# Kernel tuning notes

Measured on AMD Instinct MI355X. Metric: run time of the kernel, lower is better.

## Reference

```python
import jax, jax.numpy as jnp
import numpy as np

ALPHA = 0.2
N_ENT, N_TYP, N_REL, E = 100000, 1000, 200, 500000
D = 64          # nfeat1 = nfeat2 = nhid1 = nhid2 = relation_dim
NHEADS = 2      # forced by the tuple-unpack in the original forward


def _xavier(key, shape):
    fan_out, fan_in = shape[0], shape[-1]
    lim = 1.414 * np.sqrt(6.0 / (fan_in + fan_out))
    return jax.random.uniform(key, shape, jnp.float32, -lim, lim)


def setup_inputs() -> dict:
    key = jax.random.key(0)
    ks = jax.random.split(key, 32)
    inp = {
        "entity_embeddings": jax.random.normal(ks[0], (N_ENT, D), jnp.float32),
        "type_embed": jax.random.normal(ks[1], (N_TYP, D), jnp.float32),
        "relation_embed": jax.random.normal(ks[2], (N_REL, D), jnp.float32),
        "edge_list": jax.random.randint(ks[3], (2, E), 0, N_TYP),  # row0=src entity, row1=dst type; both in-range
        "edge_type": jax.random.randint(ks[4], (E,), 0, N_REL),
        "edge_embed": jax.random.normal(ks[5], (E, D), jnp.float32),
    }
    Din = 3 * D  # cat(x1[src], x2[dst], edge_embed)
    i = 6
    for h in range(NHEADS):
        inp[f"a_e{h}"] = _xavier(ks[i], (D, Din)); i += 1   # entity-side attention proj
        inp[f"v_e{h}"] = _xavier(ks[i], (1, D))[0]; i += 1  # entity-side score vector
        inp[f"a_t{h}"] = _xavier(ks[i], (D, Din)); i += 1   # type-side attention proj
        inp[f"v_t{h}"] = _xavier(ks[i], (1, D))[0]; i += 1
    Ho = NHEADS * D       # 128
    Dout = 3 * Ho         # out layer input cat dim
    inp["a_eo"] = _xavier(ks[i], (Ho, Dout)); i += 1
    inp["v_eo"] = _xavier(ks[i], (1, Ho))[0]; i += 1
    inp["a_to"] = _xavier(ks[i], (Ho, Dout)); i += 1
    inp["v_to"] = _xavier(ks[i], (1, Ho))[0]; i += 1
    inp["W"] = _xavier(ks[i], (D, Ho))  # relation_dim -> nheads*nhid1
    return inp


def _gat_e2t(x1, x2, src, dst, e, a_e, v_e, a_t, v_t, concat):
    """Bipartite sparse GAT layer (KBGAT-style, e2t variant).
    Message m = a @ cat(x1[src], x2[dst], edge_embed); score = exp(-leaky_relu(v . m));
    softmax-normalized scatter-aggregate to entity nodes (by src) and type nodes (by dst)."""
    d1, d2 = x1.shape[1], x2.shape[1]

    def agg(a, v, seg, nseg):
        a1, a2, a3 = a[:, :d1], a[:, d1:d1 + d2], a[:, d1 + d2:]
        # project nodes first, then gather (avoids materializing [E, 3d] cat)
        m = (x1 @ a1.T)[src] + (x2 @ a2.T)[dst] + e @ a3.T     # [E, h]
        s = jnp.exp(-jax.nn.leaky_relu(m @ v, ALPHA))          # [E] unnormalized attention
        num = jax.ops.segment_sum(m * s[:, None], seg, num_segments=nseg)
        den = jax.ops.segment_sum(s, seg, num_segments=nseg)
        h = num / jnp.where(den == 0, 1.0, den)[:, None]
        return jax.nn.elu(h) if concat else h

    h_e = agg(a_e, v_e, src, x1.shape[0])
    h_t = agg(a_t, v_t, dst, x2.shape[0])
    return h_e, h_t


def reference(entity_embeddings, type_embed, relation_embed, edge_list, edge_type, edge_embed,
              a_e0, v_e0, a_t0, v_t0, a_e1, v_e1, a_t1, v_t1,
              a_eo, v_eo, a_to, v_to, W):
    src, dst = edge_list[0], edge_list[1]
    # two attention heads (concat=True -> elu inside)
    h0e, h0t = _gat_e2t(entity_embeddings, type_embed, src, dst, edge_embed, a_e0, v_e0, a_t0, v_t0, True)
    h1e, h1t = _gat_e2t(entity_embeddings, type_embed, src, dst, edge_embed, a_e1, v_e1, a_t1, v_t1, True)
    x1 = jnp.concatenate([h0e, h1e], axis=1)  # [N_ENT, 2*nhid1]
    x2 = jnp.concatenate([h0t, h1t], axis=1)  # [N_TYP, 2*nhid2]
    # dropout is identity at inference
    out_rel = relation_embed @ W              # [N_REL, nheads*nhid1]
    e2 = out_rel[edge_type]                   # per-edge relation embedding
    o1, o2 = _gat_e2t(x1, x2, src, dst, e2, a_eo, v_eo, a_to, v_to, False)
    return jax.nn.elu(o1), jax.nn.elu(o2), out_rel
```

## Files before the change

kernel.cpp:

```cpp
#include <hip/hip_runtime.h>

#define ALPHA 0.2f
#define NT 1000
#define NRELC 200
#define NE 500000
#define N_ENT 100000
#define CH 4096
#define G 123

static constexpr size_t I_STARTS_SRC = 0;
static constexpr size_t I_STARTS_DST = 1001;
static constexpr size_t I_COLSUM     = 2002;
static constexpr size_t I_HIST2      = 4002;
static constexpr size_t I_BASE2      = 250002;
static constexpr size_t I_AB_SRC     = 496002;
static constexpr size_t I_AB_DST     = 1496002;

static constexpr size_t F_U1 = 2496004;
static constexpr size_t F_U2 = F_U1 + 768;
static constexpr size_t F_L1 = F_U2 + 768;
static constexpr size_t F_X1 = F_L1 + 4*130000;
static constexpr size_t F_X2 = F_X1 + 128000;
static constexpr size_t F_OR = F_X2 + 128000;
static constexpr size_t F_L2 = F_OR + 25600;
static constexpr size_t S2F = 283800;
static constexpr size_t WS_FLOATS = F_L2 + 2*S2F;

static constexpr size_t OUT_O2  = 12800000;
static constexpr size_t OUT_REL = 12928000;

__device__ __forceinline__ float eluf(float x) { return x > 0.f ? x : expm1f(x); }
__device__ __forceinline__ float scoref(float slin) {
  return expf(slin > 0.f ? -slin : -ALPHA * slin);
}

__global__ __launch_bounds__(256) void k_hist2(const int* __restrict__ src,
                                               const int* __restrict__ dst,
                                               int* __restrict__ ip) {
  __shared__ int h[NT];
  int bid = blockIdx.x;
  int side = bid >= G;
  int blk = bid - side * G;
  const int* keys = side ? dst : src;
  int j0 = blk * CH;
  int n = min(CH, NE - j0);
  for (int i = threadIdx.x; i < NT; i += 256) h[i] = 0;
  __syncthreads();
  for (int k = threadIdx.x; k < n; k += 256) atomicAdd(&h[keys[j0 + k]], 1);
  __syncthreads();
  int* row = ip + I_HIST2 + (size_t)(side * G + blk) * NT;
  for (int b = threadIdx.x; b < NT; b += 256) row[b] = h[b];
}

__global__ void k_colsum(int* __restrict__ ip) {
  int t = blockIdx.x * 256 + threadIdx.x;
  if (t >= 2 * NT) return;
  int side = t / NT, bin = t - side * NT;
  int s = 0;
  for (int blk = 0; blk < G; ++blk)
    s += ip[I_HIST2 + (size_t)(side * G + blk) * NT + bin];
  ip[I_COLSUM + t] = s;
}

__global__ void k_scan2b(int* __restrict__ ip) {
  __shared__ int buf[1024];
  int t = threadIdx.x;
  for (int side = 0; side < 2; ++side) {
    int v = (t < NT) ? ip[I_COLSUM + side * NT + t] : 0;
    buf[t] = v;
    __syncthreads();
    for (int off = 1; off < 1024; off <<= 1) {
      int x = (t >= off) ? buf[t - off] : 0;
      __syncthreads();
      buf[t] += x;
      __syncthreads();
    }
    int* st = ip + (side ? I_STARTS_DST : I_STARTS_SRC);
    if (t < NT) st[t] = buf[t] - v;
    if (t == NT - 1) st[NT] = buf[t];
    __syncthreads();
  }
}

__global__ void k_bases(int* __restrict__ ip) {
  int t = blockIdx.x * 256 + threadIdx.x;
  if (t >= 2 * NT) return;
  int side = t / NT, bin = t - side * NT;
  int run = ip[(side ? I_STARTS_DST : I_STARTS_SRC) + bin];
  for (int blk = 0; blk < G; ++blk) {
    size_t idx = I_HIST2 + (size_t)(side * G + blk) * NT + bin;
    int c = ip[idx];
    ip[idx + (I_BASE2 - I_HIST2)] = run;
    run += c;
  }
}

__global__ __launch_bounds__(256) void k_binscat(const int* __restrict__ src,
                                                 const int* __restrict__ dst,
                                                 const int* __restrict__ et,
                                                 int* __restrict__ ip) {
  __shared__ int2 bufs[CH];
  __shared__ int loff[1024];
  __shared__ int lcur[1024];
  __shared__ int gbase[1024];
  __shared__ int psum[256];
  int bid = blockIdx.x;
  int side = bid >= G;
  int blk = bid - side * G;
  const int* keys = side ? dst : src;
  const int* oths = side ? src : dst;
  int j0 = blk * CH;
  int n = min(CH, NE - j0);
  int t = threadIdx.x;

  for (int i = t; i < 1024; i += 256) lcur[i] = 0;
  __syncthreads();
  for (int k = t; k < n; k += 256) atomicAdd(&lcur[keys[j0 + k]], 1);
  __syncthreads();
  int c0 = lcur[4*t], c1 = lcur[4*t+1], c2 = lcur[4*t+2], c3 = lcur[4*t+3];
  int s = c0 + c1 + c2 + c3;
  psum[t] = s;
  __syncthreads();
  for (int off = 1; off < 256; off <<= 1) {
    int x = (t >= off) ? psum[t - off] : 0;
    __syncthreads();
    psum[t] += x;
    __syncthreads();
  }
  int base = psum[t] - s;
  loff[4*t]   = base;
  loff[4*t+1] = base + c0;
  loff[4*t+2] = base + c0 + c1;
  loff[4*t+3] = base + c0 + c1 + c2;
  lcur[4*t]   = loff[4*t];
  lcur[4*t+1] = loff[4*t+1];
  lcur[4*t+2] = loff[4*t+2];
  lcur[4*t+3] = loff[4*t+3];
  const int* brow = ip + I_BASE2 + (size_t)(side * G + blk) * NT;
  for (int b = t; b < NT; b += 256) gbase[b] = brow[b];
  __syncthreads();
  for (int k = t; k < n; k += 256) {
    int j = j0 + k;
    int b = keys[j];
    int pos = atomicAdd(&lcur[b], 1);
    bufs[pos] = make_int2(j | (b << 19), oths[j] | (et[j] << 16));
  }
  __syncthreads();
  int2* out = reinterpret_cast<int2*>(ip + (side ? I_AB_DST : I_AB_SRC));
  for (int k = t; k < n; k += 256) {
    int2 q = bufs[k];
    int b = q.x >> 19;
    int posg = gbase[b] + (k - loff[b]);
    out[posg] = make_int2(q.x & 0x7FFFF, q.y);
  }
}

__global__ void k_prep_u(const float* aE0, const float* vE0, const float* aT0, const float* vT0,
                         const float* aE1, const float* vE1, const float* aT1, const float* vT1,
                         const float* aEo, const float* vEo, const float* aTo, const float* vTo,
                         float* ws) {
  int t = blockIdx.x * blockDim.x + threadIdx.x;
  if (t < 768) {
    int c = t / 192, rem = t - c*192;
    int p = rem >> 6, k = rem & 63;
    const float* a = (c==0)?aE0:(c==1)?aT0:(c==2)?aE1:aT1;
    const float* v = (c==0)?vE0:(c==1)?vT0:(c==2)?vE1:vT1;
    float s = 0.f;
    for (int o = 0; o < 64; ++o) s += a[o*192 + p*64 + k] * v[o];
    ws[F_U1 + (size_t)(c*3+p)*64 + k] = s;
  } else if (t < 1536) {
    int tt = t - 768;
    int c = tt / 384, rem = tt - c*384;
    int p = rem >> 7, k = rem & 127;
    const float* a = c ? aTo : aEo;
    const float* v = c ? vTo : vEo;
    float s = 0.f;
    for (int o = 0; o < 128; ++o) s += a[o*384 + p*128 + k] * v[o];
    ws[F_U2 + (size_t)(c*3+p)*128 + k] = s;
  }
}

__global__ void k_l1_proj(const float* Ent, const float* Typ,
                          const float* aE0, const float* aT0,
                          const float* aE1, const float* aT1,
                          float* ws) {
  int stride = gridDim.x * blockDim.x;
  for (int t = blockIdx.x * blockDim.x + threadIdx.x; t < 4*130000; t += stride) {
    int c = t / 130000, rem = t - c*130000;
    const float* a = (c==0)?aE0:(c==1)?aT0:(c==2)?aE1:aT1;
    float* base = ws + F_L1 + (size_t)c * 130000;
    if (rem < 64000) {
      int i = rem >> 6, o = rem & 63;
      const float* x = Ent + (size_t)i*64;
      const float* ar = a + o*192;
      float s = 0.f;
      #pragma unroll
      for (int k = 0; k < 64; ++k) s += x[k]*ar[k];
      base[rem] = s;
    } else if (rem < 128000) {
      int rr = rem - 64000; int i = rr >> 6, o = rr & 63;
      const float* x = Typ + (size_t)i*64;
      const float* ar = a + o*192 + 64;
      float s = 0.f;
      #pragma unroll
      for (int k = 0; k < 64; ++k) s += x[k]*ar[k];
      base[64000 + rr] = s;
    } else if (rem < 129000) {
      int i = rem - 128000;
      const float* x = Ent + (size_t)i*64;
      const float* u = ws + F_U1 + (size_t)(c*3)*64;
      float s = 0.f;
      #pragma unroll
      for (int k = 0; k < 64; ++k) s += x[k]*u[k];
      base[128000 + i] = s;
    } else {
      int i = rem - 129000;
      const float* x = Typ + (size_t)i*64;
      const float* u = ws + F_U1 + (size_t)(c*3+1)*64;
      float s = 0.f;
      #pragma unroll
      for (int k = 0; k < 64; ++k) s += x[k]*u[k];
      base[129000 + i] = s;
    }
  }
}

__global__ __launch_bounds__(256) void k_l1_acc(const float* __restrict__ Eemb,
                                                const float* aE0, const float* aT0,
                                                const float* aE1, const float* aT1,
                                                const int* __restrict__ ip,
                                                float* __restrict__ ws) {
  __shared__ float Tl[2][NT];
  __shared__ float cOthL[2][NT];
  __shared__ float accR[2][16][64];
  __shared__ float accE[2][64];
  __shared__ float red[256];
  __shared__ float denl[2];

  int side = blockIdx.x >= NT;
  int g = blockIdx.x - side * NT;
  int t = threadIdx.x;
  int sub = t & 15, slot = t >> 4;
  int c0 = side, c1 = side + 2;

  size_t othOff = side ? 128000 : 129000;
  size_t ownOff = side ? 129000 : 128000;
  for (int i = t; i < NT; i += 256) {
    Tl[0][i] = 0.f; Tl[1][i] = 0.f;
    cOthL[0][i] = ws[F_L1 + (size_t)c0*130000 + othOff + i];
    cOthL[1][i] = ws[F_L1 + (size_t)c1*130000 + othOff + i];
  }
  if (t < 2) denl[t] = 0.f;
  float ownA = ws[F_L1 + (size_t)c0*130000 + ownOff + g];
  float ownB = ws[F_L1 + (size_t)c1*130000 + ownOff + g];
  float4 w3A = reinterpret_cast<const float4*>(ws + F_U1 + (size_t)(c0*3+2)*64)[sub];
  float4 w3B = reinterpret_cast<const float4*>(ws + F_U1 + (size_t)(c1*3+2)*64)[sub];
  __syncthreads();

  int start = ip[(side ? I_STARTS_DST : I_STARTS_SRC) + g];
  int end   = ip[(side ? I_STARTS_DST : I_STARTS_SRC) + g + 1];
  const int2* ab = reinterpret_cast<const int2*>(ip + (side ? I_AB_DST : I_AB_SRC));
  const float4* EV = reinterpret_cast<const float4*>(Eemb);

  float4 acc0 = make_float4(0.f,0.f,0.f,0.f);
  float4 acc1 = make_float4(0.f,0.f,0.f,0.f);
  float d0 = 0.f, d1 = 0.f;

  int p = start + slot;
  for (; p + 48 < end; p += 64) {
    int2 q0 = ab[p], q1 = ab[p+16], q2 = ab[p+32], q3 = ab[p+48];
    float4 e0 = EV[(size_t)q0.x*16 + sub];
    float4 e1 = EV[(size_t)q1.x*16 + sub];
    float4 e2 = EV[(size_t)q2.x*16 + sub];
    float4 e3 = EV[(size_t)q3.x*16 + sub];
    float rA0 = e0.x*w3A.x + e0.y*w3A.y + e0.z*w3A.z + e0.w*w3A.w;
    float rB0 = e0.x*w3B.x + e0.y*w3B.y + e0.z*w3B.z + e0.w*w3B.w;
    float rA1 = e1.x*w3A.x + e1.y*w3A.y + e1.z*w3A.z + e1.w*w3A.w;
    float rB1 = e1.x*w3B.x + e1.y*w3B.y + e1.z*w3B.z + e1.w*w3B.w;
    float rA2 = e2.x*w3A.x + e2.y*w3A.y + e2.z*w3A.z + e2.w*w3A.w;
    float rB2 = e2.x*w3B.x + e2.y*w3B.y + e2.z*w3B.z + e2.w*w3B.w;
    float rA3 = e3.x*w3A.x + e3.y*w3A.y + e3.z*w3A.z + e3.w*w3A.w;
    float rB3 = e3.x*w3B.x + e3.y*w3B.y + e3.z*w3B.z + e3.w*w3B.w;
    #pragma unroll
    for (int sh = 1; sh < 16; sh <<= 1) {
      rA0 += __shfl_xor(rA0, sh, 16); rB0 += __shfl_xor(rB0, sh, 16);
      rA1 += __shfl_xor(rA1, sh, 16); rB1 += __shfl_xor(rB1, sh, 16);
      rA2 += __shfl_xor(rA2, sh, 16); rB2 += __shfl_xor(rB2, sh, 16);
      rA3 += __shfl_xor(rA3, sh, 16); rB3 += __shfl_xor(rB3, sh, 16);
    }
    int o0 = q0.y & 0xFFFF, o1 = q1.y & 0xFFFF, o2 = q2.y & 0xFFFF, o3 = q3.y & 0xFFFF;
    float sA0 = scoref(ownA + cOthL[0][o0] + rA0);
    float sB0 = scoref(ownB + cOthL[1][o0] + rB0);
    float sA1 = scoref(ownA + cOthL[0][o1] + rA1);
    float sB1 = scoref(ownB + cOthL[1][o1] + rB1);
    float sA2 = scoref(ownA + cOthL[0][o2] + rA2);
    float sB2 = scoref(ownB + cOthL[1][o2] + rB2);
    float sA3 = scoref(ownA + cOthL[0][o3] + rA3);
    float sB3 = scoref(ownB + cOthL[1][o3] + rB3);
    acc0.x += sA0*e0.x + sA1*e1.x + sA2*e2.x + sA3*e3.x;
    acc0.y += sA0*e0.y + sA1*e1.y + sA2*e2.y + sA3*e3.y;
    acc0.z += sA0*e0.z + sA1*e1.z + sA2*e2.z + sA3*e3.z;
    acc0.w += sA0*e0.w + sA1*e1.w + sA2*e2.w + sA3*e3.w;
    acc1.x += sB0*e0.x + sB1*e1.x + sB2*e2.x + sB3*e3.x;
    acc1.y += sB0*e0.y + sB1*e1.y + sB2*e2.y + sB3*e3.y;
    acc1.z += sB0*e0.z + sB1*e1.z + sB2*e2.z + sB3*e3.z;
    acc1.w += sB0*e0.w + sB1*e1.w + sB2*e2.w + sB3*e3.w;
    if (sub == 0) {
      atomicAdd(&Tl[0][o0], sA0); atomicAdd(&Tl[1][o0], sB0);
      atomicAdd(&Tl[0][o1], sA1); atomicAdd(&Tl[1][o1], sB1);
      atomicAdd(&Tl[0][o2], sA2); atomicAdd(&Tl[1][o2], sB2);
      atomicAdd(&Tl[0][o3], sA3); atomicAdd(&Tl[1][o3], sB3);
      d0 += sA0 + sA1 + sA2 + sA3;
      d1 += sB0 + sB1 + sB2 + sB3;
    }
  }
  for (; p < end; p += 16) {
    int2 q = ab[p];
    float4 ev = EV[(size_t)q.x*16 + sub];
    float rA = ev.x*w3A.x + ev.y*w3A.y + ev.z*w3A.z + ev.w*w3A.w;
    float rB = ev.x*w3B.x + ev.y*w3B.y + ev.z*w3B.z + ev.w*w3B.w;
    #pragma unroll
    for (int sh = 1; sh < 16; sh <<= 1) {
      rA += __shfl_xor(rA, sh, 16);
      rB += __shfl_xor(rB, sh, 16);
    }
    int oth = q.y & 0xFFFF;
    float sA = scoref(ownA + cOthL[0][oth] + rA);
    float sB = scoref(ownB + cOthL[1][oth] + rB);
    acc0.x += sA*ev.x; acc0.y += sA*ev.y; acc0.z += sA*ev.z; acc0.w += sA*ev.w;
    acc1.x += sB*ev.x; acc1.y += sB*ev.y; acc1.z += sB*ev.z; acc1.w += sB*ev.w;
    if (sub == 0) {
      atomicAdd(&Tl[0][oth], sA);
      atomicAdd(&Tl[1][oth], sB);
      d0 += sA; d1 += sB;
    }
  }
  *reinterpret_cast<float4*>(&accR[0][slot][sub*4]) = acc0;
  *reinterpret_cast<float4*>(&accR[1][slot][sub*4]) = acc1;
  if (sub == 0) { atomicAdd(&denl[0], d0); atomicAdd(&denl[1], d1); }
  __syncthreads();
  if (t < 128) {
    int ci = t >> 6, o = t & 63;
    float s = 0.f;
    #pragma unroll
    for (int sl = 0; sl < 16; ++sl) s += accR[ci][sl][o];
    accE[ci][o] = s;
  }
  __syncthreads();

  int o = t & 63, part = t >> 6;
  size_t othPOff = side ? 0 : 64000;
  size_t ownPOff = side ? 64000 : 0;
  #pragma unroll
  for (int ci = 0; ci < 2; ++ci) {
    int c = side + 2*ci;
    const float* Pc = ws + F_L1 + (size_t)c * 130000;
    const float* Poth = Pc + othPOff;
    float sum = 0.f;
    for (int dd = part*250; dd < part*250 + 250; ++dd)
      sum += Tl[ci][dd] * Poth[(size_t)dd*64 + o];
    red[t] = sum;
    __syncthreads();
    if (part == 0) {
      sum = red[o] + red[64+o] + red[128+o] + red[192+o];
      const float* a = (c==0)?aE0:(c==1)?aT0:(c==2)?aE1:aT1;
      const float* a3 = a + o*192 + 128;
      float acc = 0.f;
      #pragma unroll
      for (int k = 0; k < 64; ++k) acc += accE[ci][k]*a3[k];
      float den = denl[ci];
      float own = Pc[ownPOff + (size_t)g*64 + o];
      float num = sum + acc + den*own;
      float h = num / (den == 0.f ? 1.f : den);
      float* dst = ws + (side ? F_X2 : F_X1);
      dst[(size_t)g*128 + ci*64 + o] = eluf(h);
    }
    __syncthreads();
  }
}

__global__ void k_relW(const float* Rel, const float* W, float* ws, float* dout) {
  int t = blockIdx.x * blockDim.x + threadIdx.x;
  if (t >= NRELC*128) return;
  int r = t >> 7, o = t & 127;
  const float* x = Rel + (size_t)r*64;
  float s = 0.f;
  #pragma unroll
  for (int k = 0; k < 64; ++k) s += x[k] * W[(size_t)k*128 + o];
  ws[F_OR + t] = s;
  dout[OUT_REL + t] = s;
}

__global__ void k_l2_proj(const float* aEo, const float* aTo, float* ws) {
  int stride = gridDim.x * blockDim.x;
  const float* x1 = ws + F_X1;
  const float* x2 = ws + F_X2;
  const float* orel = ws + F_OR;
  for (int t = blockIdx.x * blockDim.x + threadIdx.x; t < 2*283800; t += stride) {
    int c = t / 283800, rem = t - c*283800;
    const float* a = c ? aTo : aEo;
    float* base = ws + F_L2 + (size_t)c * S2F;
    if (rem < 128000) {
      int i = rem >> 7, o = rem & 127;
      const float* x = x1 + (size_t)i*128;
      const float* ar = a + (size_t)o*384;
      float s = 0.f;
      #pragma unroll
      for (int k = 0; k < 128; ++k) s += x[k]*ar[k];
      base[rem] = s;
    } else if (rem < 256000) {
      int rr = rem - 128000; int i = rr >> 7, o = rr & 127;
      const float* x = x2 + (size_t)i*128;
      const float* ar = a + (size_t)o*384 + 128;
      float s = 0.f;
      #pragma unroll
      for (int k = 0; k < 128; ++k) s += x[k]*ar[k];
      base[128000 + rr] = s;
    } else if (rem < 281600) {
      int rr = rem - 256000; int r = rr >> 7, o = rr & 127;
      const float* x = orel + (size_t)r*128;
      const float* ar = a + (size_t)o*384 + 256;
      float s = 0.f;
      #pragma unroll
      for (int k = 0; k < 128; ++k) s += x[k]*ar[k];
      base[256000 + rr] = s;
    } else if (rem < 282600) {
      int i = rem - 281600;
      const float* u = ws + F_U2 + (size_t)(c*3)*128;
      const float* x = x1 + (size_t)i*128;
      float s = 0.f;
      for (int k = 0; k < 128; ++k) s += x[k]*u[k];
      base[281600 + i] = s;
    } else if (rem < 283600) {
      int i = rem - 282600;
      const float* u = ws + F_U2 + (size_t)(c*3+1)*128;
      const float* x = x2 + (size_t)i*128;
      float s = 0.f;
      for (int k = 0; k < 128; ++k) s += x[k]*u[k];
      base[282600 + i] = s;
    } else {
      int r = rem - 283600;
      const float* u = ws + F_U2 + (size_t)(c*3+2)*128;
      const float* x = orel + (size_t)r*128;
      float s = 0.f;
      for (int k = 0; k < 128; ++k) s += x[k]*u[k];
      base[283600 + r] = s;
    }
  }
}

__global__ __launch_bounds__(256) void k_l2_seg(const int* __restrict__ ip,
                                                float* __restrict__ ws,
                                                float* __restrict__ dout) {
  __shared__ float Tl[NT];
  __shared__ float Ul[NRELC];
  __shared__ float cOthL[NT];
  __shared__ float cRelL[NRELC];
  __shared__ float red[256];
  __shared__ float denl;

  int c = blockIdx.x >= NT;
  int g = blockIdx.x - c * NT;
  int t = threadIdx.x;
  float* base = ws + F_L2 + (size_t)c * S2F;

  size_t othOff = c ? 281600 : 282600;
  size_t ownOff = c ? 282600 : 281600;
  for (int i = t; i < NT; i += 256) { Tl[i] = 0.f; cOthL[i] = base[othOff + i]; }
  for (int i = t; i < NRELC; i += 256) { Ul[i] = 0.f; cRelL[i] = base[283600 + i]; }
  if (t == 0) denl = 0.f;
  float own = base[ownOff + g];
  __syncthreads();

  int start = ip[(c ? I_STARTS_DST : I_STARTS_SRC) + g];
  int end   = ip[(c ? I_STARTS_DST : I_STARTS_SRC) + g + 1];
  const int2* ab = reinterpret_cast<const int2*>(ip + (c ? I_AB_DST : I_AB_SRC));

  float dpart = 0.f;
  for (int p = start + t; p < end; p += 256) {
    int2 q = ab[p];
    int oth = q.y & 0xFFFF;
    int r = q.y >> 16;
    float sv = scoref(own + cOthL[oth] + cRelL[r]);
    atomicAdd(&Tl[oth], sv);
    atomicAdd(&Ul[r], sv);
    dpart += sv;
  }
  atomicAdd(&denl, dpart);
  __syncthreads();

  int o = t & 127, part = t >> 7;
  const float* Qoth = base + (c ? 0 : 128000);
  const float* R3 = base + 256000;
  float sum = 0.f;
  for (int dd = part*500; dd < part*500 + 500; ++dd)
    sum += Tl[dd] * Qoth[(size_t)dd*128 + o];
  for (int rr = part*100; rr < part*100 + 100; ++rr)
    sum += Ul[rr] * R3[(size_t)rr*128 + o];
  red[t] = sum;
  __syncthreads();
  if (part == 0) {
    sum = red[o] + red[128+o];
    float den = denl;
    float ownQ = base[(c ? 128000 : 0) + (size_t)g*128 + o];
    float num = sum + den*ownQ;
    float h = num / (den == 0.f ? 1.f : den);
    size_t off = c ? (OUT_O2 + (size_t)g*128 + o) : ((size_t)g*128 + o);
    dout[off] = eluf(h);
  }
}

extern "C" void kernel_launch(void* const* d_in, const int* in_sizes, int n_in,
                              void* d_out, int out_size, void* d_ws, size_t ws_size,
                              hipStream_t stream) {
  (void)in_sizes; (void)n_in;
  const float* Ent = (const float*)d_in[0];
  const float* Typ = (const float*)d_in[1];
  const float* Rel = (const float*)d_in[2];
  const int*   edge = (const int*)d_in[3];
  const int*   etyp = (const int*)d_in[4];
  const float* Eemb = (const float*)d_in[5];
  const float* aE0 = (const float*)d_in[6];
  const float* vE0 = (const float*)d_in[7];
  const float* aT0 = (const float*)d_in[8];
  const float* vT0 = (const float*)d_in[9];
  const float* aE1 = (const float*)d_in[10];
  const float* vE1 = (const float*)d_in[11];
  const float* aT1 = (const float*)d_in[12];
  const float* vT1 = (const float*)d_in[13];
  const float* aEo = (const float*)d_in[14];
  const float* vEo = (const float*)d_in[15];
  const float* aTo = (const float*)d_in[16];
  const float* vTo = (const float*)d_in[17];
  const float* W   = (const float*)d_in[18];
  float* ws  = (float*)d_ws;
  int*   ip  = (int*)d_ws;
  float* out = (float*)d_out;
  const int* srcA = edge;
  const int* dstA = edge + NE;

  if (ws_size < WS_FLOATS * sizeof(float)) return;

  hipMemsetAsync(d_out, 0, (size_t)out_size * sizeof(float), stream);

  k_hist2  <<<2*G, 256, 0, stream>>>(srcA, dstA, ip);
  k_colsum <<<8, 256, 0, stream>>>(ip);
  k_scan2b <<<1, 1024, 0, stream>>>(ip);
  k_bases  <<<8, 256, 0, stream>>>(ip);
  k_binscat<<<2*G, 256, 0, stream>>>(srcA, dstA, etyp, ip);
  k_prep_u <<<6, 256, 0, stream>>>(aE0,vE0,aT0,vT0,aE1,vE1,aT1,vT1,aEo,vEo,aTo,vTo,ws);
  k_l1_proj<<<2048, 256, 0, stream>>>(Ent, Typ, aE0, aT0, aE1, aT1, ws);
  k_l1_acc <<<2000, 256, 0, stream>>>(Eemb, aE0, aT0, aE1, aT1, ip, ws);
  k_relW   <<<100, 256, 0, stream>>>(Rel, W, ws, out);
  k_l2_proj<<<2218, 256, 0, stream>>>(aEo, aTo, ws);
  k_l2_seg <<<2000, 256, 0, stream>>>(ip, ws, out);
}
```

Before: 303.6 us.

## Tile node projection kernels with shared-memory row tiles and register blocking

Rewrites the layer-1 and layer-2 node projection kernels so that each block stages a 16-row tile of node features in shared memory. Each thread then computes 4 or 8 output rows for one output column, reusing each weight element across those rows. The scalar u-vector dot products move to a separate tail range of blocks. This is meant to cut redundant global loads of features and weights, at the cost of fewer blocks and more register pressure.

Result: faster. 262.5 us (-13.6%).

```diff
diff --git a/kernel.cpp b/kernel.cpp
--- a/kernel.cpp
+++ b/kernel.cpp
@@ -180,41 +180,56 @@
   }
 }
 
-__global__ void k_l1_proj(const float* Ent, const float* Typ,
-                          const float* aE0, const float* aT0,
-                          const float* aE1, const float* aT1,
-                          float* ws) {
-  int stride = gridDim.x * blockDim.x;
-  for (int t = blockIdx.x * blockDim.x + threadIdx.x; t < 4*130000; t += stride) {
-    int c = t / 130000, rem = t - c*130000;
+__global__ __launch_bounds__(256) void k_l1_proj(const float* Ent, const float* Typ,
+                                                 const float* aE0, const float* aT0,
+                                                 const float* aE1, const float* aT1,
+                                                 float* ws) {
+  int bid = blockIdx.x;
+  int t = threadIdx.x;
+  if (bid < 504) {
+    __shared__ float xs[16][64];
+    int c = bid / 126, rem = bid - c*126;
+    int table = rem / 63, tile = rem - table*63;
+    int i0 = tile * 16;
     const float* a = (c==0)?aE0:(c==1)?aT0:(c==2)?aE1:aT1;
+    const float* x = table ? Typ : Ent;
+    float* outb = ws + F_L1 + (size_t)c*130000 + (table ? 64000 : 0);
+    for (int idx = t; idx < 1024; idx += 256) {
+      int r = idx >> 6, k = idx & 63;
+      int i = i0 + r;
+      xs[r][k] = (i < NT) ? x[(size_t)i*64 + k] : 0.f;
+    }
+    __syncthreads();
+    int o = t & 63, grp = t >> 6;
+    const float* arow = a + o*192 + table*64;
+    float acc0 = 0.f, acc1 = 0.f, acc2 = 0.f, acc3 = 0.f;
+    #pragma unroll 8
+    for (int k = 0; k < 64; ++k) {
+      float av = arow[k];
+      acc0 += xs[grp*4+0][k] * av;
+      acc1 += xs[grp*4+1][k] * av;
+      acc2 += xs[grp*4+2][k] * av;
+      acc3 += xs[grp*4+3][k] * av;
+    }
+    int ib = i0 + grp*4;
+    if (ib + 0 < NT) outb[(size_t)(ib+0)*64 + o] = acc0;
+    if (ib + 1 < NT) outb[(size_t)(ib+1)*64 + o] = acc1;
+    if (ib + 2 < NT) outb[(size_t)(ib+2)*64 + o] = acc2;
+    if (ib + 3 < NT) outb[(size_t)(ib+3)*64 + o] = acc3;
+  } else {
+    int idx = (bid - 504) * 256 + t;
+    if (idx >= 8000) return;
+    int c = idx / 2000, rem = idx - c*2000;
     float* base = ws + F_L1 + (size_t)c * 130000;
-    if (rem < 64000) {
-      int i = rem >> 6, o = rem & 63;
-      const float* x = Ent + (size_t)i*64;
-      const float* ar = a + o*192;
-      float s = 0.f;
-      #pragma unroll
-      for (int k = 0; k < 64; ++k) s += x[k]*ar[k];
-      base[rem] = s;
-    } else if (rem < 128000) {
-      int rr = rem - 64000; int i = rr >> 6, o = rr & 63;
-      const float* x = Typ + (size_t)i*64;
-      const float* ar = a + o*192 + 64;
-      float s = 0.f;
-      #pragma unroll
-      for (int k = 0; k < 64; ++k) s += x[k]*ar[k];
-      base[64000 + rr] = s;
-    } else if (rem < 129000) {
-      int i = rem - 128000;
-      const float* x = Ent + (size_t)i*64;
+    if (rem < 1000) {
+      const float* x = Ent + (size_t)rem*64;
       const float* u = ws + F_U1 + (size_t)(c*3)*64;
       float s = 0.f;
       #pragma unroll
       for (int k = 0; k < 64; ++k) s += x[k]*u[k];
-      base[128000 + i] = s;
+      base[128000 + rem] = s;
     } else {
-      int i = rem - 129000;
+      int i = rem - 1000;
       const float* x = Typ + (size_t)i*64;
       const float* u = ws + F_U1 + (size_t)(c*3+1)*64;
       float s = 0.f;
@@ -391,55 +406,63 @@
   dout[OUT_REL + t] = s;
 }
 
-__global__ void k_l2_proj(const float* aEo, const float* aTo, float* ws) {
-  int stride = gridDim.x * blockDim.x;
+__global__ __launch_bounds__(256) void k_l2_proj(const float* aEo, const float* aTo,
+                                                 float* ws) {
+  int bid = blockIdx.x;
+  int t = threadIdx.x;
   const float* x1 = ws + F_X1;
   const float* x2 = ws + F_X2;
   const float* orel = ws + F_OR;
-  for (int t = blockIdx.x * blockDim.x + threadIdx.x; t < 2*283800; t += stride) {
-    int c = t / 283800, rem = t - c*283800;
+  if (bid < 278) {
+    __shared__ float xs[16][128];
+    int c = bid / 139, rem = bid - c*139;
     const float* a = c ? aTo : aEo;
+    float* cb = ws + F_L2 + (size_t)c * S2F;
+    const float* x; int part, tile, nrows; float* outb;
+    if (rem < 63)       { x = x1;   part = 0; tile = rem;       nrows = NT;    outb = cb; }
+    else if (rem < 126) { x = x2;   part = 1; tile = rem - 63;  nrows = NT;    outb = cb + 128000; }
+    else                { x = orel; part = 2; tile = rem - 126; nrows = NRELC; outb = cb + 256000; }
+    int i0 = tile * 16;
+    for (int idx = t; idx < 2048; idx += 256) {
+      int r = idx >> 7, k = idx & 127;
+      int i = i0 + r;
+      xs[r][k] = (i < nrows) ? x[(size_t)i*128 + k] : 0.f;
+    }
+    __syncthreads();
+    int o = t & 127, grp = t >> 7;
+    const float* arow = a + (size_t)o*384 + part*128;
+    float acc[8] = {0.f,0.f,0.f,0.f,0.f,0.f,0.f,0.f};
+    #pragma unroll 4
+    for (int k = 0; k < 128; ++k) {
+      float av = arow[k];
+      #pragma unroll
+      for (int r = 0; r < 8; ++r)
+        acc[r] += xs[grp*8+r][k] * av;
+    }
+    int ib = i0 + grp*8;
+    #pragma unroll
+    for (int r = 0; r < 8; ++r)
+      if (ib + r < nrows) outb[(size_t)(ib+r)*128 + o] = acc[r];
+  } else {
+    int idx = (bid - 278) * 256 + t;
+    if (idx >= 4400) return;
+    int c = idx / 2200, rem = idx - c*2200;
     float* base = ws + F_L2 + (size_t)c * S2F;
-    if (rem < 128000) {
-      int i = rem >> 7, o = rem & 127;
-      const float* x = x1 + (size_t)i*128;
-      const float* ar = a + (size_t)o*384;
-      float s = 0.f;
-      #pragma unroll
-      for (int k = 0; k < 128; ++k) s += x[k]*ar[k];
-      base[rem] = s;
-    } else if (rem < 256000) {
-      int rr = rem - 128000; int i = rr >> 7, o = rr & 127;
-      const float* x = x2 + (size_t)i*128;
-      const float* ar = a + (size_t)o*384 + 128;
-      float s = 0.f;
-      #pragma unroll
-      for (int k = 0; k < 128; ++k) s += x[k]*ar[k];
-      base[128000 + rr] = s;
-    } else if (rem < 281600) {
-      int rr = rem - 256000; int r = rr >> 7, o = rr & 127;
-      const float* x = orel + (size_t)r*128;
-      const float* ar = a + (size_t)o*384 + 256;
-      float s = 0.f;
-      #pragma unroll
-      for (int k = 0; k < 128; ++k) s += x[k]*ar[k];
-      base[256000 + rr] = s;
-    } else if (rem < 282600) {
-      int i = rem - 281600;
+    if (rem < 1000) {
       const float* u = ws + F_U2 + (size_t)(c*3)*128;
-      const float* x = x1 + (size_t)i*128;
+      const float* x = x1 + (size_t)rem*128;
       float s = 0.f;
       for (int k = 0; k < 128; ++k) s += x[k]*u[k];
-      base[281600 + i] = s;
-    } else if (rem < 283600) {
-      int i = rem - 282600;
+      base[281600 + rem] = s;
+    } else if (rem < 2000) {
+      int i = rem - 1000;
       const float* u = ws + F_U2 + (size_t)(c*3+1)*128;
       const float* x = x2 + (size_t)i*128;
       float s = 0.f;
       for (int k = 0; k < 128; ++k) s += x[k]*u[k];
       base[282600 + i] = s;
     } else {
-      int r = rem - 283600;
+      int r = rem - 2000;
       const float* u = ws + F_U2 + (size_t)(c*3+2)*128;
       const float* x = orel + (size_t)r*128;
       float s = 0.f;
@@ -549,9 +572,9 @@
   k_bases  <<<8, 256, 0, stream>>>(ip);
   k_binscat<<<2*G, 256, 0, stream>>>(srcA, dstA, etyp, ip);
   k_prep_u <<<6, 256, 0, stream>>>(aE0,vE0,aT0,vT0,aE1,vE1,aT1,vT1,aEo,vEo,aTo,vTo,ws);
-  k_l1_proj<<<2048, 256, 0, stream>>>(Ent, Typ, aE0, aT0, aE1, aT1, ws);
+  k_l1_proj<<<536, 256, 0, stream>>>(Ent, Typ, aE0, aT0, aE1, aT1, ws);
   k_l1_acc <<<2000, 256, 0, stream>>>(Eemb, aE0, aT0, aE1, aT1, ip, ws);
   k_relW   <<<100, 256, 0, stream>>>(Rel, W, ws, out);
-  k_l2_proj<<<2218, 256, 0, stream>>>(aEo, aTo, ws);
+  k_l2_proj<<<296, 256, 0, stream>>>(aEo, aTo, ws);
   k_l2_seg <<<2000, 256, 0, stream>>>(ip, ws, out);
 }
```
